# Optimization experiments

Hardware: AMD Instinct MI355X
Metric: run time of the kernel (lower is better)

The kernel has to match this reference:

```python
import jax, jax.numpy as jnp
import numpy as np

B, N, D = 32, 2048, 1024


def setup_inputs() -> dict:
    key = jax.random.key(0)
    k1, k2, k3, k4, k5, k6 = jax.random.split(key, 6)
    encoded = jax.random.normal(k1, (B, N, D), dtype=jnp.float32)
    decoder_state = jax.random.normal(k2, (B, D), dtype=jnp.float32)
    mask = jax.random.randint(k3, (B, N), 0, 2, dtype=jnp.int32)
    scale = 1.0 / np.sqrt(D)
    W1 = jax.random.normal(k4, (D, D), dtype=jnp.float32) * scale  # applied as x @ W1
    W2 = jax.random.normal(k5, (D, D), dtype=jnp.float32) * scale
    vt = jax.random.normal(k6, (D,), dtype=jnp.float32) * scale
    return {"encoded": encoded, "decoder_state": decoder_state, "mask": mask,
            "W1": W1, "W2": W2, "vt": vt}


def reference(encoded, decoder_state, mask, W1, W2, vt):
    temperature = 1.0
    # process_encoded: W1(encoded)  [B, N, D]
    enc = jnp.einsum('bnd,de->bne', encoded, W1)
    # W2(decoder_state)  [B, D] -> broadcast-add over N
    dec = decoder_state @ W2
    # vt(tanh(.)).squeeze(2)  -> logits [B, N]
    u = jnp.einsum('bnd,d->bn', jnp.tanh(enc + dec[:, None, :]), vt)
    # masked log-softmax with temperature over dim=1
    logits = u / temperature + jnp.log(mask.astype(u.dtype) + 1e-45)
    return jax.nn.log_softmax(logits, axis=1)
```

## Files before the change

### kernel.cpp

```cpp
#include <hip/hip_runtime.h>

typedef _Float16 half8 __attribute__((ext_vector_type(8)));
typedef __fp16   pk2   __attribute__((ext_vector_type(2)));
typedef float    f32x4 __attribute__((ext_vector_type(4)));

#define GLOBAL_AS __attribute__((address_space(1)))
#define LDS_AS    __attribute__((address_space(3)))

static constexpr int Bb = 32;
static constexpr int Nn = 2048;
static constexpr int Dd = 1024;
static constexpr int M  = Bb * Nn;


__global__ void prep_w1(const float* __restrict__ W1, _Float16* __restrict__ W1TT) {
    int g = blockIdx.x * 256 + threadIdx.x;
    int chunk = g >> 10;
    int u = g & 1023;
    int q = u >> 7, sc = u & 127;
    int cl = sc ^ (2 * (q & 3));
    int et = chunk >> 5, t = (chunk >> 1) & 15, h = chunk & 1;
    int e  = et * 256 + h * 128 + cl;
    int k0 = t * 64 + q * 8;
    half8 hh;
#pragma unroll
    for (int j = 0; j < 8; ++j)
        hh[j] = (_Float16)W1[(size_t)(k0 + j) * Dd + e];
    *(half8*)(W1TT + (size_t)g * 8) = hh;
}

__global__ void prep_enc(const float* __restrict__ A, _Float16* __restrict__ A_p) {
    __shared__ _Float16 T[128 * 64];
    const int c = blockIdx.x;
    const int tid = threadIdx.x;
    const int mtile = c >> 5, t = (c >> 1) & 15, h = c & 1;
    const int r = tid >> 1, kh = tid & 1;
    const float* src = A + (size_t)(mtile * 256 + h * 128 + r) * Dd + t * 64 + kh * 32;
    const int rx = r & 7;
#pragma unroll
    for (int i = 0; i < 4; ++i) {
        f32x4 a  = *(const f32x4*)(src + i * 8);
        f32x4 b2 = *(const f32x4*)(src + i * 8 + 4);
        half8 hh; pk2 p;
        p = __builtin_amdgcn_cvt_pkrtz(a.x, a.y);   hh[0] = p[0]; hh[1] = p[1];
        p = __builtin_amdgcn_cvt_pkrtz(a.z, a.w);   hh[2] = p[0]; hh[3] = p[1];
        p = __builtin_amdgcn_cvt_pkrtz(b2.x, b2.y); hh[4] = p[0]; hh[5] = p[1];
        p = __builtin_amdgcn_cvt_pkrtz(b2.z, b2.w); hh[6] = p[0]; hh[7] = p[1];
        *(half8*)(T + r * 64 + (((kh * 4 + i) ^ rx) * 8)) = hh;
    }
    __syncthreads();
    const size_t cb = (size_t)c * 8192;
#pragma unroll
    for (int i = 0; i < 4; ++i) {
        int u = i * 256 + tid;
        int q = u >> 7, sr = u & 127;
        int lr = sr ^ (2 * (q & 3));
        half8 hh = *(const half8*)(T + lr * 64 + ((q ^ (lr & 7)) * 8));
        *(half8*)(A_p + cb + (size_t)u * 8) = hh;
    }
}

__global__ void dec_kernel(const float* __restrict__ ds, const float* __restrict__ W2,
                           float* __restrict__ dec) {
    __shared__ float part[4][64];
    int b = blockIdx.x, ech = blockIdx.y;
    int tid = threadIdx.x;
    int e = ech * 64 + (tid & 63);
    int dc = tid >> 6;
    float acc = 0.f;
#pragma unroll 4
    for (int d = dc * 256; d < dc * 256 + 256; ++d)
        acc += ds[b * Dd + d] * W2[(size_t)d * Dd + e];
    part[dc][tid & 63] = acc;
    __syncthreads();
    if (tid < 64)
        dec[b * Dd + e] = part[0][tid] + part[1][tid] + part[2][tid] + part[3][tid];
}

#define BAR     asm volatile("s_barrier" ::: "memory")
#define LGKM(n) asm volatile("s_waitcnt lgkmcnt(" #n ")" ::: "memory")
#define VM(n)   asm volatile("s_waitcnt vmcnt(" #n ")" ::: "memory")
#define PRIO1   __builtin_amdgcn_s_setprio(1)
#define PRIO0   __builtin_amdgcn_s_setprio(0)

#define RD_A(dst, base) do { _Pragma("unroll") \
  for (int ks = 0; ks < 2; ++ks) { const int qb = ((ks * 4 + qq) * 128) * 8; \
    _Pragma("unroll") for (int m2 = 0; m2 < 4; ++m2) \
      dst[m2][ks] = *(const half8*)&lds[(base) + qb + (m2 * 32 + rA) * 8]; } } while (0)

#define RD_B(dst, base) do { _Pragma("unroll") \
  for (int ks = 0; ks < 2; ++ks) { const int qb = ((ks * 4 + qq) * 128) * 8; \
    _Pragma("unroll") for (int j2 = 0; j2 < 2; ++j2) \
      dst[j2][ks] = *(const half8*)&lds[(base) + qb + (j2 * 64 + rB) * 8]; } } while (0)

#define MFMAQ(A_, B_, ro, co) do { \
  _Pragma("unroll") for (int m2 = 0; m2 < 4; ++m2) \
  _Pragma("unroll") for (int j2 = 0; j2 < 2; ++j2) { \
    acc[(ro) + m2][(co) + j2] = __builtin_amdgcn_mfma_f32_16x16x32_f16( \
        A_[m2][0], B_[j2][0], acc[(ro) + m2][(co) + j2], 0, 0, 0); \
    acc[(ro) + m2][(co) + j2] = __builtin_amdgcn_mfma_f32_16x16x32_f16( \
        A_[m2][1], B_[j2][1], acc[(ro) + m2][(co) + j2], 0, 0, 0); } } while (0)

__global__ __launch_bounds__(512) void gemm8(
    const _Float16* __restrict__ A_p, const _Float16* __restrict__ W1TT,
    const float* __restrict__ dec, const float* __restrict__ vt,
    float* __restrict__ u_part)
{
    extern __shared__ _Float16 lds[];

    const int g  = blockIdx.x;
    const int wg = (g & 7) * 128 + (g >> 3);
    const int et    = wg & 3;
    const int mtile = wg >> 2;

    const int tid  = threadIdx.x;
    const int lane = tid & 63, wid = tid >> 6;
    const int wr = wid >> 2, wc = wid & 3;
    const int qq = lane >> 4, l15 = lane & 15;
    const int l15s = l15 ^ (2 * qq);
    const int rA = wr * 16 + l15s;
    const int rB = wc * 16 + l15s;

    f32x4 acc[8][4] = {};
    half8 a[4][2], b0[2][2], b1[2][2];

    const size_t abase = (size_t)mtile * 32 * 8192;
    const size_t bbase = (size_t)et * 32 * 8192;
    const int uoff = tid * 8;

    auto stA = [&](int T, int h) {
        const _Float16* gp = A_p + abase + ((size_t)(T * 2 + h) << 13) + uoff;
        _Float16* lp = lds + ((((T & 1) * 2 + h) << 13) + (wid << 9));
        __builtin_amdgcn_global_load_lds((const GLOBAL_AS void*)gp,
                                         (LDS_AS void*)lp, 16, 0, 0);
        __builtin_amdgcn_global_load_lds((const GLOBAL_AS void*)(gp + 4096),
                                         (LDS_AS void*)(lp + 4096), 16, 0, 0);
    };
    auto stB = [&](int T, int h) {
        const _Float16* gp = W1TT + bbase + ((size_t)(T * 2 + h) << 13) + uoff;
        _Float16* lp = lds + (32768 + (((T & 1) * 2 + h) << 13) + (wid << 9));
        __builtin_amdgcn_global_load_lds((const GLOBAL_AS void*)gp,
                                         (LDS_AS void*)lp, 16, 0, 0);
        __builtin_amdgcn_global_load_lds((const GLOBAL_AS void*)(gp + 4096),
                                         (LDS_AS void*)(lp + 4096), 16, 0, 0);
    };


    stA(0, 0); stB(0, 0); stB(0, 1); stA(0, 1);
    VM(2);
    BAR;

#pragma unroll 1
    for (int i = 0; i < 8; ++i) {
        const int E = 2 * i, O = E + 1;
        const bool s = (i < 7);

        RD_A(a, 0);
        RD_B(b0, 32768);
        RD_B(b1, 40960);
        stA(O, 0); stB(O, 0); stB(O, 1);
        BAR; LGKM(0);
        PRIO1; MFMAQ(a, b0, 0, 0); MFMAQ(a, b1, 0, 2); PRIO0;
        VM(6);
        BAR;

        RD_A(a, 8192);
        stA(O, 1);
        BAR; LGKM(0);
        PRIO1; MFMAQ(a, b0, 4, 0); MFMAQ(a, b1, 4, 2); PRIO0;
        VM(2);
        BAR;

        RD_A(a, 16384);
        RD_B(b0, 49152);
        RD_B(b1, 57344);
        if (s) { stA(E + 2, 0); stB(E + 2, 0); stB(E + 2, 1); }
        BAR; LGKM(0);
        PRIO1; MFMAQ(a, b0, 0, 0); MFMAQ(a, b1, 0, 2); PRIO0;
        if (s) { VM(6); } else { VM(0); }
        BAR;

        RD_A(a, 24576);
        if (s) stA(E + 2, 1);
        BAR; LGKM(0);
        PRIO1; MFMAQ(a, b0, 4, 0); MFMAQ(a, b1, 4, 2); PRIO0;
        VM(2);
        BAR;
    }

    const int b = mtile >> 3;
    float vtv[4], dcv[4];
#pragma unroll
    for (int nf = 0; nf < 4; ++nf) {
        int e = et * 256 + (nf >> 1) * 128 + (nf & 1) * 64 + wc * 16 + l15;
        vtv[nf] = vt[e];
        dcv[nf] = dec[b * Dd + e];
    }
    float* usum = (float*)lds;
#pragma unroll
    for (int hm = 0; hm < 8; ++hm) {
        const int h = hm >> 2, mq = hm & 3;
#pragma unroll
        for (int r = 0; r < 4; ++r) {
            float sv = 0.f;
#pragma unroll
            for (int nf = 0; nf < 4; ++nf) {
                float x  = acc[hm][nf][r] + dcv[nf];
                float ex = __expf(2.f * x);
                sv += (1.f - 2.f * __builtin_amdgcn_rcpf(ex + 1.f)) * vtv[nf];
            }
#pragma unroll
            for (int off = 1; off < 16; off <<= 1) sv += __shfl_xor(sv, off, 16);
            if (l15 == 0)
                usum[wc * 256 + h * 128 + mq * 32 + wr * 16 + qq * 4 + r] = sv;
        }
    }
    __syncthreads();
    if (tid < 256) {
        float v = usum[tid] + usum[256 + tid] + usum[512 + tid] + usum[768 + tid];
        u_part[(size_t)et * M + (size_t)mtile * 256 + tid] = v;
    }
}

__global__ void softmax_k(const float* __restrict__ up, const int* __restrict__ mask,
                          float* __restrict__ out) {
    __shared__ float red[8];
    int b = blockIdx.x, tid = threadIdx.x;
    float l[8];
#pragma unroll
    for (int i = 0; i < 8; ++i) {
        int n = i * 256 + tid;
        float s = up[(size_t)b * Nn + n];
#pragma unroll
        for (int et = 1; et < 4; ++et) s += up[(size_t)et * M + (size_t)b * Nn + n];
        l[i] = s + (mask[b * Nn + n] ? 0.f : -103.278931f);
    }
    float m = l[0];
#pragma unroll
    for (int i = 1; i < 8; ++i) m = fmaxf(m, l[i]);
#pragma unroll
    for (int o = 32; o >= 1; o >>= 1) m = fmaxf(m, __shfl_xor(m, o, 64));
    if ((tid & 63) == 0) red[tid >> 6] = m;
    __syncthreads();
    m = fmaxf(fmaxf(red[0], red[1]), fmaxf(red[2], red[3]));
    float s = 0.f;
#pragma unroll
    for (int i = 0; i < 8; ++i) s += expf(l[i] - m);
#pragma unroll
    for (int o = 32; o >= 1; o >>= 1) s += __shfl_xor(s, o, 64);
    if ((tid & 63) == 0) red[4 + (tid >> 6)] = s;
    __syncthreads();
    float lse = m + logf(red[4] + red[5] + red[6] + red[7]);
#pragma unroll
    for (int i = 0; i < 8; ++i)
        out[(size_t)b * Nn + i * 256 + tid] = l[i] - lse;
}

extern "C" void kernel_launch(void* const* d_in, const int* in_sizes, int n_in,
                              void* d_out, int out_size, void* d_ws, size_t ws_size,
                              hipStream_t stream) {
    const float* encoded = (const float*)d_in[0];
    const float* dstate  = (const float*)d_in[1];
    const int*   mask    = (const int*)d_in[2];
    const float* W1      = (const float*)d_in[3];
    const float* W2      = (const float*)d_in[4];
    const float* vt      = (const float*)d_in[5];
    float* out = (float*)d_out;

    char* ws = (char*)d_ws;
    float*    u_part = (float*)ws;
    float*    dec    = (float*)(ws + (size_t)4 * M * 4);
    _Float16* W1TT   = (_Float16*)(ws + (size_t)4 * M * 4 + (size_t)Bb * Dd * 4);
    _Float16* A_p    = (_Float16*)(ws + (size_t)4 * M * 4 + (size_t)Bb * Dd * 4
                                   + (size_t)Dd * Dd * 2);

    static bool attr_done = false;
    if (!attr_done) {
        hipFuncSetAttribute(reinterpret_cast<const void*>(gemm8),
                            hipFuncAttributeMaxDynamicSharedMemorySize, 131072);
        attr_done = true;
    }

    prep_w1<<<512, 256, 0, stream>>>(W1, W1TT);
    dec_kernel<<<dim3(32, 16), 256, 0, stream>>>(dstate, W2, dec);
    prep_enc<<<8192, 256, 0, stream>>>(encoded, A_p);
    gemm8<<<1024, 512, 131072, stream>>>(A_p, W1TT, dec, vt, u_part);
    softmax_k<<<32, 256, 0, stream>>>(u_part, mask, out);
}
```

Baseline: 565.6 us.

## Restructure GEMM main loop into single-barrier double-buffered K steps

Replaces the four-phase-per-iteration schedule, which had several barriers and partial vmcnt waits, with one step per K tile. Each step issues all global-to-LDS loads for the next tile, reads both A halves and B into separate register sets, and uses staged lgkmcnt waits so MFMAs can start while LDS reads are still arriving, then does one full vmcnt wait and a barrier. The enc prep kernel also now loads rows with coalesced float4 reads across 16 threads per row and writes half4 into the swizzled LDS tile. The new loop cuts barrier count but waits on all outstanding global loads each step and holds more registers.

```diff
diff --git a/kernel.cpp b/kernel.cpp
--- a/kernel.cpp
+++ b/kernel.cpp
@@ -1,6 +1,7 @@
 #include <hip/hip_runtime.h>
 
 typedef _Float16 half8 __attribute__((ext_vector_type(8)));
+typedef _Float16 half4 __attribute__((ext_vector_type(4)));
 typedef __fp16   pk2   __attribute__((ext_vector_type(2)));
 typedef float    f32x4 __attribute__((ext_vector_type(4)));
 
@@ -34,28 +35,27 @@
     const int c = blockIdx.x;
     const int tid = threadIdx.x;
     const int mtile = c >> 5, t = (c >> 1) & 15, h = c & 1;
-    const int r = tid >> 1, kh = tid & 1;
-    const float* src = A + (size_t)(mtile * 256 + h * 128 + r) * Dd + t * 64 + kh * 32;
-    const int rx = r & 7;
-#pragma unroll
-    for (int i = 0; i < 4; ++i) {
-        f32x4 a  = *(const f32x4*)(src + i * 8);
-        f32x4 b2 = *(const f32x4*)(src + i * 8 + 4);
-        half8 hh; pk2 p;
-        p = __builtin_amdgcn_cvt_pkrtz(a.x, a.y);   hh[0] = p[0]; hh[1] = p[1];
-        p = __builtin_amdgcn_cvt_pkrtz(a.z, a.w);   hh[2] = p[0]; hh[3] = p[1];
-        p = __builtin_amdgcn_cvt_pkrtz(b2.x, b2.y); hh[4] = p[0]; hh[5] = p[1];
-        p = __builtin_amdgcn_cvt_pkrtz(b2.z, b2.w); hh[6] = p[0]; hh[7] = p[1];
-        *(half8*)(T + r * 64 + (((kh * 4 + i) ^ rx) * 8)) = hh;
+    const int r0 = tid >> 4, ks = tid & 15;
+    const int q = ks >> 1, h4 = ks & 1;
+    const float* src0 = A + (size_t)(mtile * 256 + h * 128 + r0) * Dd
+                          + t * 64 + ks * 4;
+#pragma unroll
+    for (int p = 0; p < 8; ++p) {
+        const int r = p * 16 + r0;
+        f32x4 a = *(const f32x4*)(src0 + (size_t)p * 16 * Dd);
+        pk2 p0 = __builtin_amdgcn_cvt_pkrtz(a.x, a.y);
+        pk2 p1 = __builtin_amdgcn_cvt_pkrtz(a.z, a.w);
+        half4 hh; hh[0] = p0[0]; hh[1] = p0[1]; hh[2] = p1[0]; hh[3] = p1[1];
+        *(half4*)(T + r * 64 + ((q ^ (r & 7)) * 8) + h4 * 4) = hh;
     }
     __syncthreads();
     const size_t cb = (size_t)c * 8192;
 #pragma unroll
     for (int i = 0; i < 4; ++i) {
         int u = i * 256 + tid;
-        int q = u >> 7, sr = u & 127;
-        int lr = sr ^ (2 * (q & 3));
-        half8 hh = *(const half8*)(T + lr * 64 + ((q ^ (lr & 7)) * 8));
+        int qq2 = u >> 7, sr = u & 127;
+        int lr = sr ^ (2 * (qq2 & 3));
+        half8 hh = *(const half8*)(T + lr * 64 + ((qq2 ^ (lr & 7)) * 8));
         *(half8*)(A_p + cb + (size_t)u * 8) = hh;
     }
 }
@@ -122,7 +122,7 @@
     const int rB = wc * 16 + l15s;
 
     f32x4 acc[8][4] = {};
-    half8 a[4][2], b0[2][2], b1[2][2];
+    half8 ax[4][2], ay[4][2], b0[2][2], b1[2][2];
 
     const size_t abase = (size_t)mtile * 32 * 8192;
     const size_t bbase = (size_t)et * 32 * 8192;
@@ -146,45 +146,31 @@
     };
 
 
-    stA(0, 0); stB(0, 0); stB(0, 1); stA(0, 1);
-    VM(2);
+    stA(0, 0); stA(0, 1); stB(0, 0); stB(0, 1);
+    VM(0);
     BAR;
 
-#pragma unroll 1
-    for (int i = 0; i < 8; ++i) {
-        const int E = 2 * i, O = E + 1;
-        const bool s = (i < 7);
-
-        RD_A(a, 0);
-        RD_B(b0, 32768);
-        RD_B(b1, 40960);
-        stA(O, 0); stB(O, 0); stB(O, 1);
-        BAR; LGKM(0);
-        PRIO1; MFMAQ(a, b0, 0, 0); MFMAQ(a, b1, 0, 2); PRIO0;
-        VM(6);
-        BAR;
-
-        RD_A(a, 8192);
-        stA(O, 1);
-        BAR; LGKM(0);
-        PRIO1; MFMAQ(a, b0, 4, 0); MFMAQ(a, b1, 4, 2); PRIO0;
-        VM(2);
-        BAR;
-
-        RD_A(a, 16384);
-        RD_B(b0, 49152);
-        RD_B(b1, 57344);
-        if (s) { stA(E + 2, 0); stB(E + 2, 0); stB(E + 2, 1); }
-        BAR; LGKM(0);
-        PRIO1; MFMAQ(a, b0, 0, 0); MFMAQ(a, b1, 0, 2); PRIO0;
-        if (s) { VM(6); } else { VM(0); }
-        BAR;
-
-        RD_A(a, 24576);
-        if (s) stA(E + 2, 1);
-        BAR; LGKM(0);
-        PRIO1; MFMAQ(a, b0, 4, 0); MFMAQ(a, b1, 4, 2); PRIO0;
-        VM(2);
+#pragma unroll 2
+    for (int T = 0; T < 16; ++T) {
+        const int As  = (T & 1) << 14;
+        const int Bs2 = 32768 + ((T & 1) << 14);
+        const bool s = (T < 15);
+
+        if (s) { stA(T + 1, 0); stA(T + 1, 1); stB(T + 1, 0); stB(T + 1, 1); }
+
+        RD_A(ax, As);
+        RD_B(b0, Bs2);
+        RD_B(b1, Bs2 + 8192);
+        RD_A(ay, As + 8192);
+
+        LGKM(12);
+        PRIO1; MFMAQ(ax, b0, 0, 0); PRIO0;
+        LGKM(8);
+        PRIO1; MFMAQ(ax, b1, 0, 2); PRIO0;
+        LGKM(0);
+        PRIO1; MFMAQ(ay, b0, 4, 0); MFMAQ(ay, b1, 4, 2); PRIO0;
+
+        VM(0);
         BAR;
     }
 
```

New measurement: 554.5 us. -2.0%, faster.
